# Kernel optimization log

Hardware: AMD Instinct MI355X
Metric: run time of the kernel (lower is better)

The kernel has to match this reference:

```python
import jax, jax.numpy as jnp
import numpy as np

T, H, F, E, TOP_K = 2048, 1024, 4096, 8, 2


def setup_inputs() -> dict:
    key = jax.random.key(0)
    k0, k1, k2, k3, k4 = jax.random.split(key, 5)
    return {
        "hidden_states": jax.random.normal(k0, (T, H), dtype=jnp.float32),
        "gate_w": jax.random.normal(k1, (E, H), dtype=jnp.float32) * 0.02,  # [E, H] (out, in)
        "w1": jax.random.normal(k2, (E, F, H), dtype=jnp.float32) * 0.02,
        "w2": jax.random.normal(k3, (E, H, F), dtype=jnp.float32) * 0.02,
        "w3": jax.random.normal(k4, (E, F, H), dtype=jnp.float32) * 0.02,
    }


def reference(hidden_states, gate_w, w1, w2, w3):
    # Router: logits -> soft-capped tanh -> fp32 softmax -> top-k
    logits = hidden_states @ gate_w.T                       # [T, E]
    logits = 30.0 * jnp.tanh(logits / 30.0)
    probs = jax.nn.softmax(logits.astype(jnp.float32), axis=-1)
    vals, idx = jax.lax.top_k(probs, TOP_K)                 # [T, K]
    vals = vals.astype(hidden_states.dtype)
    # combine[t, e] = sum_k vals[t, k] * (idx[t, k] == e)
    combine = jnp.sum(
        jax.nn.one_hot(idx, E, dtype=vals.dtype) * vals[..., None], axis=1
    )                                                       # [T, E]
    # Per-expert SwiGLU-style MLP (GELU gate), computed densely and combined
    # with routing weights (zero weight == token not routed to expert).
    g = jax.nn.gelu(jnp.einsum('th,efh->etf', hidden_states, w1), approximate=False)
    u = jnp.einsum('th,efh->etf', hidden_states, w3)        # [E, T, F]
    out = jnp.einsum('etf,ehf->eth', g * u, w2)             # [E, T, H]
    return jnp.einsum('eth,te->th', out, combine)           # [T, H]
```

## Files before the change

### kernel.cpp

```cpp
#include <hip/hip_runtime.h>
#include <hip/hip_bf16.h>

#define TT 2048
#define HH 1024
#define FF 4096
#define NE 8
#define BK 64

typedef __attribute__((ext_vector_type(4))) float f4;
typedef __attribute__((ext_vector_type(4))) short s4;
typedef __attribute__((ext_vector_type(8))) short s8;

static __device__ __forceinline__ short f2bf(float x) {
  union { __hip_bfloat16 b; short s; } u;
  u.b = __float2bfloat16(x);
  return u.s;
}

static __device__ __forceinline__ void gload16(const void* g, void* l) {
  __builtin_amdgcn_global_load_lds(
      (const __attribute__((address_space(1))) void*)g,
      (__attribute__((address_space(3))) void*)l, 16, 0, 0);
}

__global__ __launch_bounds__(256) void k_cvt(
    const float* __restrict__ src, __hip_bfloat16* __restrict__ dst, int n8)
{
  int i = blockIdx.x * blockDim.x + threadIdx.x;
  const int stride = gridDim.x * blockDim.x;
  for (; i < n8; i += stride) {
    f4 a = ((const f4*)src)[2 * i];
    f4 b = ((const f4*)src)[2 * i + 1];
    s8 o = { f2bf(a.x), f2bf(a.y), f2bf(a.z), f2bf(a.w),
             f2bf(b.x), f2bf(b.y), f2bf(b.z), f2bf(b.w) };
    ((s8*)dst)[i] = o;
  }
}

__global__ __launch_bounds__(256) void k_router(
    const float* __restrict__ h, const float* __restrict__ gw,
    int* __restrict__ cnt, int* __restrict__ tok, float* __restrict__ wt)
{
  const int lane = threadIdx.x & 63;
  const int wid  = threadIdx.x >> 6;
  const int t = blockIdx.x * 4 + wid;
  const float* hr = h + (size_t)t * HH;

  float acc[NE];
#pragma unroll
  for (int e = 0; e < NE; e++) acc[e] = 0.f;
#pragma unroll 4
  for (int i = 0; i < HH / 64; i++) {
    float hv = hr[lane + (i << 6)];
#pragma unroll
    for (int e = 0; e < NE; e++) acc[e] += hv * gw[e * HH + lane + (i << 6)];
  }
#pragma unroll
  for (int e = 0; e < NE; e++) {
    float v = acc[e];
#pragma unroll
    for (int s = 32; s > 0; s >>= 1) v += __shfl_xor(v, s);
    acc[e] = v;
  }
  if (lane == 0) {
    float p[NE];
    float m = -1e30f;
#pragma unroll
    for (int e = 0; e < NE; e++) {
      p[e] = 30.f * tanhf(acc[e] * (1.f / 30.f));
      m = fmaxf(m, p[e]);
    }
    float s = 0.f;
#pragma unroll
    for (int e = 0; e < NE; e++) { p[e] = expf(p[e] - m); s += p[e]; }
    const float inv = 1.f / s;
    int e1 = 0;
#pragma unroll
    for (int e = 1; e < NE; e++) if (p[e] > p[e1]) e1 = e;
    int e2 = (e1 == 0) ? 1 : 0;
#pragma unroll
    for (int e = 0; e < NE; e++) if (e != e1 && p[e] > p[e2]) e2 = e;

    int pos1 = atomicAdd(&cnt[e1], 1);
    tok[e1 * TT + pos1] = t;
    wt [e1 * TT + pos1] = p[e1] * inv;
    int pos2 = atomicAdd(&cnt[e2], 1);
    tok[e2 * TT + pos2] = t;
    wt [e2 * TT + pos2] = p[e2] * inv;
  }
}

template<bool GPASS>
__global__ __launch_bounds__(256) void k_ffn1(
    const __hip_bfloat16* __restrict__ hb, const __hip_bfloat16* __restrict__ wb,
    const int* __restrict__ cnt, const int* __restrict__ tok,
    __hip_bfloat16* __restrict__ act)
{
  const int e  = blockIdx.z;
  const int mt = blockIdx.y;
  const int nt = blockIdx.x;
  const int ce = cnt[e];
  if (mt * 128 >= ce) return;
  int base = 0;
  for (int i = 0; i < e; i++) base += cnt[i];

  __shared__ short As[128 * BK];
  __shared__ short Bs[128 * BK];

  const int tid  = threadIdx.x;
  const int lane = tid & 63;
  const int wid  = tid >> 6;
  const int wm   = wid >> 1;
  const int wn   = wid & 1;

  const int srow = (wid << 3) + (lane >> 3);
  const int scol = (lane & 7) << 3;
  const __hip_bfloat16* asrc[4];
#pragma unroll
  for (int i = 0; i < 4; i++) {
    int pos = mt * 128 + i * 32 + srow;
    int tk  = tok[e * TT + min(pos, ce - 1)];
    asrc[i] = hb + (size_t)tk * HH + scol;
  }
  const __hip_bfloat16* bsrc[4];
#pragma unroll
  for (int i = 0; i < 4; i++) {
    int fr = nt * 128 + i * 32 + srow;
    bsrc[i] = wb + ((size_t)e * FF + fr) * HH + scol;
  }

  f4 acc[4][4];
#pragma unroll
  for (int i = 0; i < 4; i++)
#pragma unroll
    for (int j = 0; j < 4; j++) { f4 z = {0.f,0.f,0.f,0.f}; acc[i][j] = z; }

  for (int kk = 0; kk < HH; kk += BK) {
#pragma unroll
    for (int i = 0; i < 4; i++) {
      gload16(asrc[i] + kk, &As[(i * 32 + (wid << 3)) * BK]);
      gload16(bsrc[i] + kk, &Bs[(i * 32 + (wid << 3)) * BK]);
    }
    __syncthreads();
#pragma unroll
    for (int ks = 0; ks < 2; ks++) {
      const int ko = ks * 32 + ((lane >> 4) << 3);
      s8 af[4], bf_[4];
#pragma unroll
      for (int i = 0; i < 4; i++)
        af[i]  = *(const s8*)&As[(wm * 64 + i * 16 + (lane & 15)) * BK + ko];
#pragma unroll
      for (int j = 0; j < 4; j++)
        bf_[j] = *(const s8*)&Bs[(wn * 64 + j * 16 + (lane & 15)) * BK + ko];
#pragma unroll
      for (int i = 0; i < 4; i++)
#pragma unroll
        for (int j = 0; j < 4; j++)
          acc[i][j] = __builtin_amdgcn_mfma_f32_16x16x32_bf16(af[i], bf_[j], acc[i][j], 0, 0, 0);
    }
    __syncthreads();
  }

  const int orow0 = wm * 64 + ((lane >> 4) << 2);
  const int ocol0 = nt * 128 + wn * 64 + (lane & 15);
#pragma unroll
  for (int i = 0; i < 4; i++)
#pragma unroll
    for (int r = 0; r < 4; r++) {
      int rr = mt * 128 + orow0 + i * 16 + r;
      if (rr < ce) {
        size_t rowoff = (size_t)(base + rr) * FF + ocol0;
#pragma unroll
        for (int j = 0; j < 4; j++) {
          float v = acc[i][j][r];
          if (GPASS) {
            float u = __bfloat162float(act[rowoff + j * 16]);
            v = 0.5f * v * (1.f + erff(v * 0.70710678118f)) * u;
          }
          act[rowoff + j * 16] = __float2bfloat16(v);
        }
      }
    }
}

__global__ __launch_bounds__(256) void k_ffn2(
    const __hip_bfloat16* __restrict__ act, const __hip_bfloat16* __restrict__ w2b,
    const int* __restrict__ cnt, const int* __restrict__ tok,
    const float* __restrict__ wt, float* __restrict__ out)
{
  const int e  = blockIdx.z >> 2;
  const int sk = blockIdx.z & 3;
  const int mt = blockIdx.y;
  const int nt = blockIdx.x;
  const int ce = cnt[e];
  if (mt * 128 >= ce) return;
  int base = 0;
  for (int i = 0; i < e; i++) base += cnt[i];

  __shared__ short As[128 * BK];
  __shared__ short Bs[128 * BK];

  const int tid  = threadIdx.x;
  const int lane = tid & 63;
  const int wid  = tid >> 6;
  const int wm   = wid >> 1;
  const int wn   = wid & 1;

  const int srow = (wid << 3) + (lane >> 3);
  const int scol = (lane & 7) << 3;
  const __hip_bfloat16* asrc[4];
#pragma unroll
  for (int i = 0; i < 4; i++) {
    int pos = mt * 128 + i * 32 + srow;
    int rc  = min(pos, ce - 1);
    asrc[i] = act + (size_t)(base + rc) * FF + (sk << 10) + scol;
  }
  const __hip_bfloat16* bsrc[4];
#pragma unroll
  for (int i = 0; i < 4; i++) {
    int hr = nt * 128 + i * 32 + srow;
    bsrc[i] = w2b + ((size_t)e * HH + hr) * FF + (sk << 10) + scol;
  }

  f4 acc[4][4];
#pragma unroll
  for (int i = 0; i < 4; i++)
#pragma unroll
    for (int j = 0; j < 4; j++) { f4 z = {0.f,0.f,0.f,0.f}; acc[i][j] = z; }

  for (int kk = 0; kk < 1024; kk += BK) {
#pragma unroll
    for (int i = 0; i < 4; i++) {
      gload16(asrc[i] + kk, &As[(i * 32 + (wid << 3)) * BK]);
      gload16(bsrc[i] + kk, &Bs[(i * 32 + (wid << 3)) * BK]);
    }
    __syncthreads();
#pragma unroll
    for (int ks = 0; ks < 2; ks++) {
      const int ko = ks * 32 + ((lane >> 4) << 3);
      s8 af[4], bf_[4];
#pragma unroll
      for (int i = 0; i < 4; i++)
        af[i]  = *(const s8*)&As[(wm * 64 + i * 16 + (lane & 15)) * BK + ko];
#pragma unroll
      for (int j = 0; j < 4; j++)
        bf_[j] = *(const s8*)&Bs[(wn * 64 + j * 16 + (lane & 15)) * BK + ko];
#pragma unroll
      for (int i = 0; i < 4; i++)
#pragma unroll
        for (int j = 0; j < 4; j++)
          acc[i][j] = __builtin_amdgcn_mfma_f32_16x16x32_bf16(af[i], bf_[j], acc[i][j], 0, 0, 0);
    }
    __syncthreads();
  }

  const int orow0 = wm * 64 + ((lane >> 4) << 2);
  const int ocol0 = nt * 128 + wn * 64 + (lane & 15);
#pragma unroll
  for (int i = 0; i < 4; i++)
#pragma unroll
    for (int r = 0; r < 4; r++) {
      int rr = mt * 128 + orow0 + i * 16 + r;
      if (rr < ce) {
        int   tkn = tok[e * TT + rr];
        float w   = wt [e * TT + rr];
        float* orow = out + (size_t)tkn * HH + ocol0;
#pragma unroll
        for (int j = 0; j < 4; j++)
          atomicAdd(&orow[j * 16], acc[i][j][r] * w);
      }
    }
}

extern "C" void kernel_launch(void* const* d_in, const int* in_sizes, int n_in,
                              void* d_out, int out_size, void* d_ws, size_t ws_size,
                              hipStream_t stream)
{
  (void)in_sizes; (void)n_in; (void)ws_size;
  const float* h  = (const float*)d_in[0];
  const float* gw = (const float*)d_in[1];
  const float* w1 = (const float*)d_in[2];
  const float* w2 = (const float*)d_in[3];
  const float* w3 = (const float*)d_in[4];
  float* out = (float*)d_out;

  char* ws = (char*)d_ws;
  int*   cnt = (int*)ws;
  int*   tok = (int*)(ws + 1024);
  float* wtp = (float*)(ws + 1024 + 65536);
  __hip_bfloat16* act = (__hip_bfloat16*)(ws + 262144);
  __hip_bfloat16* hb  = (__hip_bfloat16*)(ws + 262144 + 33554432);
  __hip_bfloat16* w1b = hb  + (size_t)TT * HH;
  __hip_bfloat16* w3b = w1b + (size_t)NE * FF * HH;
  __hip_bfloat16* w2b = w3b + (size_t)NE * FF * HH;

  hipMemsetAsync(cnt, 0, 32, stream);
  hipMemsetAsync(d_out, 0, (size_t)out_size * sizeof(float), stream);

  k_cvt<<<dim3(1024), dim3(256), 0, stream>>>(h,  hb,  TT * HH / 8);
  k_cvt<<<dim3(2048), dim3(256), 0, stream>>>(w1, w1b, NE * FF * HH / 8);
  k_cvt<<<dim3(2048), dim3(256), 0, stream>>>(w3, w3b, NE * FF * HH / 8);
  k_cvt<<<dim3(2048), dim3(256), 0, stream>>>(w2, w2b, NE * HH * FF / 8);

  k_router<<<dim3(TT / 4), dim3(256), 0, stream>>>(h, gw, cnt, tok, wtp);

  k_ffn1<false><<<dim3(FF / 128, 16, NE), dim3(256), 0, stream>>>(hb, w3b, cnt, tok, act);
  k_ffn1<true ><<<dim3(FF / 128, 16, NE), dim3(256), 0, stream>>>(hb, w1b, cnt, tok, act);
  k_ffn2<<<dim3(HH / 128, 16, NE * 4), dim3(256), 0, stream>>>(act, w2b, cnt, tok, wtp, out);
}
```

Before: 743.0 us.

## Double-buffer LDS tiles with XOR swizzle in expert GEMMs, widen convert grids

Both expert GEMM kernels now use two LDS buffers and prefetch the next K tile with direct global-to-LDS loads while MFMAs run on the current one. A partial vmcnt wait plus raw barriers replaces the per-iteration __syncthreads. The LDS column index is XOR-swizzled by row to cut bank conflicts on fragment reads. The fp32-to-bf16 weight conversion launches use twice as many blocks. LDS use doubles, which may lower occupancy, and the hand-written vmcnt count depends on exactly eight loads being issued per stage.

```diff
diff --git a/kernel.cpp b/kernel.cpp
--- a/kernel.cpp
+++ b/kernel.cpp
@@ -90,6 +90,8 @@
   }
 }
 
+#define SWZCOL(l) (((((l) & 7) ^ (((l) >> 3) & 7))) << 3)
+
 template<bool GPASS>
 __global__ __launch_bounds__(256) void k_ffn1(
     const __hip_bfloat16* __restrict__ hb, const __hip_bfloat16* __restrict__ wb,
@@ -104,8 +106,8 @@
   int base = 0;
   for (int i = 0; i < e; i++) base += cnt[i];
 
-  __shared__ short As[128 * BK];
-  __shared__ short Bs[128 * BK];
+  __shared__ short As[2][128 * BK];
+  __shared__ short Bs[2][128 * BK];
 
   const int tid  = threadIdx.x;
   const int lane = tid & 63;
@@ -114,7 +116,7 @@
   const int wn   = wid & 1;
 
   const int srow = (wid << 3) + (lane >> 3);
-  const int scol = (lane & 7) << 3;
+  const int scol = SWZCOL(lane);
   const __hip_bfloat16* asrc[4];
 #pragma unroll
   for (int i = 0; i < 4; i++) {
@@ -135,30 +137,50 @@
 #pragma unroll
     for (int j = 0; j < 4; j++) { f4 z = {0.f,0.f,0.f,0.f}; acc[i][j] = z; }
 
-  for (int kk = 0; kk < HH; kk += BK) {
-#pragma unroll
-    for (int i = 0; i < 4; i++) {
-      gload16(asrc[i] + kk, &As[(i * 32 + (wid << 3)) * BK]);
-      gload16(bsrc[i] + kk, &Bs[(i * 32 + (wid << 3)) * BK]);
-    }
-    __syncthreads();
+#define STAGE1(kk, b)                                                  \
+  {                                                                    \
+    _Pragma("unroll")                                                  \
+    for (int i_ = 0; i_ < 4; i_++) {                                   \
+      gload16(asrc[i_] + (kk), &As[b][(i_ * 32 + (wid << 3)) * BK]);   \
+      gload16(bsrc[i_] + (kk), &Bs[b][(i_ * 32 + (wid << 3)) * BK]);   \
+    }                                                                  \
+  }
+
+  const int xorv = lane & 7;
+  const int hi   = lane >> 4;
+  const int frow = lane & 15;
+
+  STAGE1(0, 0);
+  int cur = 0;
+  const int NT = HH / BK;
+  for (int t = 0; t < NT; t++) {
+    if (t + 1 < NT) {
+      STAGE1((t + 1) * BK, cur ^ 1);
+      asm volatile("s_waitcnt vmcnt(8)" ::: "memory");
+    } else {
+      asm volatile("s_waitcnt vmcnt(0)" ::: "memory");
+    }
+    __builtin_amdgcn_s_barrier();
+    __builtin_amdgcn_sched_barrier(0);
 #pragma unroll
     for (int ks = 0; ks < 2; ks++) {
-      const int ko = ks * 32 + ((lane >> 4) << 3);
+      const int col = (((ks << 2) + hi) ^ xorv) << 3;
       s8 af[4], bf_[4];
 #pragma unroll
       for (int i = 0; i < 4; i++)
-        af[i]  = *(const s8*)&As[(wm * 64 + i * 16 + (lane & 15)) * BK + ko];
+        af[i]  = *(const s8*)&As[cur][(wm * 64 + i * 16 + frow) * BK + col];
 #pragma unroll
       for (int j = 0; j < 4; j++)
-        bf_[j] = *(const s8*)&Bs[(wn * 64 + j * 16 + (lane & 15)) * BK + ko];
+        bf_[j] = *(const s8*)&Bs[cur][(wn * 64 + j * 16 + frow) * BK + col];
 #pragma unroll
       for (int i = 0; i < 4; i++)
 #pragma unroll
         for (int j = 0; j < 4; j++)
           acc[i][j] = __builtin_amdgcn_mfma_f32_16x16x32_bf16(af[i], bf_[j], acc[i][j], 0, 0, 0);
     }
-    __syncthreads();
+    __builtin_amdgcn_sched_barrier(0);
+    __builtin_amdgcn_s_barrier();
+    cur ^= 1;
   }
 
   const int orow0 = wm * 64 + ((lane >> 4) << 2);
@@ -197,8 +219,8 @@
   int base = 0;
   for (int i = 0; i < e; i++) base += cnt[i];
 
-  __shared__ short As[128 * BK];
-  __shared__ short Bs[128 * BK];
+  __shared__ short As[2][128 * BK];
+  __shared__ short Bs[2][128 * BK];
 
   const int tid  = threadIdx.x;
   const int lane = tid & 63;
@@ -207,7 +229,7 @@
   const int wn   = wid & 1;
 
   const int srow = (wid << 3) + (lane >> 3);
-  const int scol = (lane & 7) << 3;
+  const int scol = SWZCOL(lane);
   const __hip_bfloat16* asrc[4];
 #pragma unroll
   for (int i = 0; i < 4; i++) {
@@ -228,30 +250,41 @@
 #pragma unroll
     for (int j = 0; j < 4; j++) { f4 z = {0.f,0.f,0.f,0.f}; acc[i][j] = z; }
 
-  for (int kk = 0; kk < 1024; kk += BK) {
-#pragma unroll
-    for (int i = 0; i < 4; i++) {
-      gload16(asrc[i] + kk, &As[(i * 32 + (wid << 3)) * BK]);
-      gload16(bsrc[i] + kk, &Bs[(i * 32 + (wid << 3)) * BK]);
-    }
-    __syncthreads();
+  const int xorv = lane & 7;
+  const int hi   = lane >> 4;
+  const int frow = lane & 15;
+
+  STAGE1(0, 0);
+  int cur = 0;
+  const int NT = 1024 / BK;
+  for (int t = 0; t < NT; t++) {
+    if (t + 1 < NT) {
+      STAGE1((t + 1) * BK, cur ^ 1);
+      asm volatile("s_waitcnt vmcnt(8)" ::: "memory");
+    } else {
+      asm volatile("s_waitcnt vmcnt(0)" ::: "memory");
+    }
+    __builtin_amdgcn_s_barrier();
+    __builtin_amdgcn_sched_barrier(0);
 #pragma unroll
     for (int ks = 0; ks < 2; ks++) {
-      const int ko = ks * 32 + ((lane >> 4) << 3);
+      const int col = (((ks << 2) + hi) ^ xorv) << 3;
       s8 af[4], bf_[4];
 #pragma unroll
       for (int i = 0; i < 4; i++)
-        af[i]  = *(const s8*)&As[(wm * 64 + i * 16 + (lane & 15)) * BK + ko];
+        af[i]  = *(const s8*)&As[cur][(wm * 64 + i * 16 + frow) * BK + col];
 #pragma unroll
       for (int j = 0; j < 4; j++)
-        bf_[j] = *(const s8*)&Bs[(wn * 64 + j * 16 + (lane & 15)) * BK + ko];
+        bf_[j] = *(const s8*)&Bs[cur][(wn * 64 + j * 16 + frow) * BK + col];
 #pragma unroll
       for (int i = 0; i < 4; i++)
 #pragma unroll
         for (int j = 0; j < 4; j++)
           acc[i][j] = __builtin_amdgcn_mfma_f32_16x16x32_bf16(af[i], bf_[j], acc[i][j], 0, 0, 0);
     }
-    __syncthreads();
+    __builtin_amdgcn_sched_barrier(0);
+    __builtin_amdgcn_s_barrier();
+    cur ^= 1;
   }
 
   const int orow0 = wm * 64 + ((lane >> 4) << 2);
@@ -298,9 +331,9 @@
   hipMemsetAsync(d_out, 0, (size_t)out_size * sizeof(float), stream);
 
   k_cvt<<<dim3(1024), dim3(256), 0, stream>>>(h,  hb,  TT * HH / 8);
-  k_cvt<<<dim3(2048), dim3(256), 0, stream>>>(w1, w1b, NE * FF * HH / 8);
-  k_cvt<<<dim3(2048), dim3(256), 0, stream>>>(w3, w3b, NE * FF * HH / 8);
-  k_cvt<<<dim3(2048), dim3(256), 0, stream>>>(w2, w2b, NE * HH * FF / 8);
+  k_cvt<<<dim3(4096), dim3(256), 0, stream>>>(w1, w1b, NE * FF * HH / 8);
+  k_cvt<<<dim3(4096), dim3(256), 0, stream>>>(w3, w3b, NE * FF * HH / 8);
+  k_cvt<<<dim3(4096), dim3(256), 0, stream>>>(w2, w2b, NE * HH * FF / 8);
 
   k_router<<<dim3(TT / 4), dim3(256), 0, stream>>>(h, gw, cnt, tok, wtp);
 
```

Measured after the change: 715.9 us. 3.7% less time.
